# Kernel optimization log

Measured on AMD Instinct MI355X. Metric: run time of the kernel, lower is better.

Reference implementation:

```python
import jax, jax.numpy as jnp
import numpy as np

N = 20000      # nodes
E = 320000     # edges (before self-loops)
IN = 256       # in_channels
HID = 64       # hidden_channels
HEADS = 4      # num_heads
OUT = 64       # out_channels
NEG_SLOPE = 0.2  # GATConv default leaky-relu slope


def setup_inputs() -> dict:
    key = jax.random.key(0)
    ks = jax.random.split(key, 12)
    s = 0.1
    x = jax.random.normal(ks[0], (N, IN), dtype=jnp.float32)
    edge_index = jax.random.randint(ks[1], (2, E), 0, N, dtype=jnp.int64)
    # Layer 1: IN -> HID per head, HEADS heads, concat
    W1 = jax.random.normal(ks[2], (IN, HEADS * HID), dtype=jnp.float32) * s
    a1_src = jax.random.normal(ks[3], (HEADS, HID), dtype=jnp.float32) * s
    a1_dst = jax.random.normal(ks[4], (HEADS, HID), dtype=jnp.float32) * s
    b1 = jnp.zeros((HEADS * HID,), dtype=jnp.float32)
    # Layer 2: HEADS*HID -> OUT, 1 head, no concat
    W2 = jax.random.normal(ks[5], (HEADS * HID, OUT), dtype=jnp.float32) * s
    a2_src = jax.random.normal(ks[6], (1, OUT), dtype=jnp.float32) * s
    a2_dst = jax.random.normal(ks[7], (1, OUT), dtype=jnp.float32) * s
    b2 = jnp.zeros((OUT,), dtype=jnp.float32)
    return {"x": x, "edge_index": edge_index,
            "W1": W1, "a1_src": a1_src, "a1_dst": a1_dst, "b1": b1,
            "W2": W2, "a2_src": a2_src, "a2_dst": a2_dst, "b2": b2}


def _gat_layer(x, src, dst, W, a_src, a_dst, bias, heads, out_c, concat):
    n = x.shape[0]
    h = (x @ W).reshape(n, heads, out_c)                    # [N,H,C]
    e_src = jnp.einsum('nhc,hc->nh', h, a_src)              # [N,H]
    e_dst = jnp.einsum('nhc,hc->nh', h, a_dst)              # [N,H]
    logits = jax.nn.leaky_relu(e_src[src] + e_dst[dst], NEG_SLOPE)  # [E',H]
    # segment softmax over incoming edges of each dst node
    m = jax.ops.segment_max(logits, dst, num_segments=n)    # [N,H]
    p = jnp.exp(logits - m[dst])                            # [E',H]
    z = jax.ops.segment_sum(p, dst, num_segments=n)         # [N,H]
    alpha = p / z[dst]                                      # [E',H]
    out = jax.ops.segment_sum(h[src] * alpha[:, :, None], dst, num_segments=n)
    out = out.reshape(n, heads * out_c) if concat else out.mean(axis=1)
    return out + bias


def reference(x, edge_index, W1, a1_src, a1_dst, b1, W2, a2_src, a2_dst, b2):
    # PyG GATConv adds self-loops by default
    loop = jnp.arange(N, dtype=edge_index.dtype)
    src = jnp.concatenate([edge_index[0], loop])
    dst = jnp.concatenate([edge_index[1], loop])
    h = _gat_layer(x, src, dst, W1, a1_src, a1_dst, b1, HEADS, HID, True)
    h = jax.nn.elu(h)
    # F.dropout defaults training=False -> identity in eval reference
    out = _gat_layer(h, src, dst, W2, a2_src, a2_dst, b2, 1, OUT, False)
    return out
```

## Files before the change

### kernel.cpp

```cpp
#include <hip/hip_runtime.h>
#include <math.h>

#define NEG 0.2f
#define CSTRIDE 64
#define LOG2E 1.4426950408889634f

typedef __attribute__((ext_vector_type(8))) short bf16x8;
typedef __attribute__((ext_vector_type(4))) float f32x4;
typedef unsigned int u32;

__device__ inline float bf2f(unsigned short u) {
    union { unsigned int i; float f; } v; v.i = ((unsigned int)u) << 16; return v.f;
}
__device__ inline unsigned short f2bf(float f) {
    union { float f; unsigned int i; } v; v.f = f;
    unsigned int r = v.i + 0x7FFF + ((v.i >> 16) & 1);
    return (unsigned short)(r >> 16);
}
__device__ inline void unpack8(uint4 hv, float* o) {
    o[0] = bf2f((unsigned short)(hv.x & 0xffffu));
    o[1] = bf2f((unsigned short)(hv.x >> 16));
    o[2] = bf2f((unsigned short)(hv.y & 0xffffu));
    o[3] = bf2f((unsigned short)(hv.y >> 16));
    o[4] = bf2f((unsigned short)(hv.z & 0xffffu));
    o[5] = bf2f((unsigned short)(hv.z >> 16));
    o[6] = bf2f((unsigned short)(hv.w & 0xffffu));
    o[7] = bf2f((unsigned short)(hv.w >> 16));
}
__device__ inline void load_lds16(const unsigned short* g, unsigned short* l) {
    __builtin_amdgcn_global_load_lds((const __attribute__((address_space(1))) u32*)g,
                                     (__attribute__((address_space(3))) u32*)l, 16, 0, 0);
}

__device__ void gemm1_block(int bm, int bn, unsigned short* As, unsigned short* Bs,
                            const unsigned short* __restrict__ A,
                            const unsigned short* __restrict__ Bt,
                            unsigned short* __restrict__ C,
                            const float* __restrict__ a1s, const float* __restrict__ a1d,
                            float* __restrict__ es, float* __restrict__ ed, int M) {
    const int tid = threadIdx.x;
    const int wave = tid >> 6, lane = tid & 63;
    const int wm = (wave >> 1) * 64, wn = (wave & 1) * 64;
    const int lm = lane & 15, kq = lane >> 4;
    const int rA = lane >> 2, cA = (lane & 3) * 8;

    int grA[2], grB[2];
#pragma unroll
    for (int i = 0; i < 2; ++i) {
        int c = wave * 2 + i;
        int gr = bm + c * 16 + rA;
        if (gr >= M) gr = M - 1;
        grA[i] = gr;
        grB[i] = bn + c * 16 + rA;
    }

    auto stage = [&](int t, int b) {
        const int k0 = t * 32;
        const int ka = (k0 < 512) ? k0 : k0 - 512;
#pragma unroll
        for (int i = 0; i < 2; ++i) {
            int c = wave * 2 + i;
            load_lds16(A + (size_t)grA[i] * 512 + ka + cA, As + b * 4096 + c * 512);
            load_lds16(Bt + (size_t)grB[i] * 768 + k0 + cA, Bs + b * 4096 + c * 512);
        }
    };

    f32x4 acc[4][4] = {};
    stage(0, 0);
    stage(1, 1);
    int buf = 0;
    for (int t = 0; t < 24; ++t) {
        if (t < 22) {
            int nb = buf + 2;
            if (nb >= 3) nb -= 3;
            stage(t + 2, nb);
            asm volatile("s_waitcnt vmcnt(8)" ::: "memory");
        } else if (t == 22) {
            asm volatile("s_waitcnt vmcnt(4)" ::: "memory");
        } else {
            asm volatile("s_waitcnt vmcnt(0)" ::: "memory");
        }
        __builtin_amdgcn_s_barrier();
        __builtin_amdgcn_sched_barrier(0);
        bf16x8 af[4], bfr[4];
#pragma unroll
        for (int f = 0; f < 4; ++f) af[f] = *(const bf16x8*)(As + buf * 4096 + (wm + f * 16 + lm) * 32 + kq * 8);
#pragma unroll
        for (int f = 0; f < 4; ++f) bfr[f] = *(const bf16x8*)(Bs + buf * 4096 + (wn + f * 16 + lm) * 32 + kq * 8);
#pragma unroll
        for (int fr = 0; fr < 4; ++fr)
#pragma unroll
            for (int fc = 0; fc < 4; ++fc)
                acc[fr][fc] = __builtin_amdgcn_mfma_f32_16x16x32_bf16(af[fr], bfr[fc], acc[fr][fc], 0, 0, 0);
        __builtin_amdgcn_s_barrier();
        __builtin_amdgcn_sched_barrier(0);
        buf = (buf + 1 == 3) ? 0 : buf + 1;
    }
    const int head = (bn + wn) >> 6;
    float asv[4], adv[4];
#pragma unroll
    for (int fc = 0; fc < 4; ++fc) {
        int ch = fc * 16 + lm;
        asv[fc] = a1s[head * 64 + ch];
        adv[fc] = a1d[head * 64 + ch];
    }
#pragma unroll
    for (int fr = 0; fr < 4; ++fr)
#pragma unroll
        for (int i = 0; i < 4; ++i) {
            int row = bm + wm + fr * 16 + kq * 4 + i;
            float se = 0.f, de = 0.f;
#pragma unroll
            for (int fc = 0; fc < 4; ++fc) {
                float c = acc[fr][fc][i];
                se = fmaf(asv[fc], c, se);
                de = fmaf(adv[fc], c, de);
            }
#pragma unroll
            for (int off = 1; off < 16; off <<= 1) {
                se += __shfl_xor(se, off, 64);
                de += __shfl_xor(de, off, 64);
            }
            if (row < M) {
                if (lm == 0) {
                    es[row * 4 + head] = se * LOG2E;
                    ed[row * 4 + head] = de * LOG2E;
                }
#pragma unroll
                for (int fc = 0; fc < 4; ++fc)
                    C[(size_t)row * 256 + bn + wn + fc * 16 + lm] = f2bf(acc[fr][fc][i]);
            }
        }
}

__global__ __launch_bounds__(256) void pre(const float* __restrict__ x,
                                           const float* __restrict__ W1,
                                           const float* __restrict__ W2,
                                           unsigned short* __restrict__ xs,
                                           unsigned short* __restrict__ Wt1,
                                           unsigned short* __restrict__ Wt2,
                                           int* __restrict__ cnt,
                                           int xb, int wb, int N) {
    int b = blockIdx.x, tid = threadIdx.x;
    if (b < xb) {
        int i = b * 256 + tid;
        if (i >= N * 64) return;
        int e0 = i * 4;
        int node = e0 >> 8, c = e0 & 255;
        float4 f = *(const float4*)(x + e0);
        unsigned short h0 = f2bf(f.x), h1 = f2bf(f.y), h2 = f2bf(f.z), h3 = f2bf(f.w);
        uint2 hi, lo;
        hi.x = (u32)h0 | ((u32)h1 << 16);
        hi.y = (u32)h2 | ((u32)h3 << 16);
        lo.x = (u32)f2bf(f.x - bf2f(h0)) | ((u32)f2bf(f.y - bf2f(h1)) << 16);
        lo.y = (u32)f2bf(f.z - bf2f(h2)) | ((u32)f2bf(f.w - bf2f(h3)) << 16);
        *(uint2*)(xs + (size_t)node * 512 + c) = hi;
        *(uint2*)(xs + (size_t)node * 512 + 256 + c) = lo;
    } else if (b < xb + wb) {
        int i = (b - xb) * 256 + tid;
        const float* W;
        unsigned short* Wt;
        int outc;
        if (i < 256 * 768) { W = W1; Wt = Wt1; outc = 256; }
        else {
            i -= 256 * 768;
            if (i >= 64 * 768) return;
            W = W2; Wt = Wt2; outc = 64;
        }
        int n = i / 768, k = i % 768;
        int ksrc = (k < 256) ? k : (k < 512 ? k - 256 : k - 512);
        float f = W[(size_t)ksrc * outc + n];
        unsigned short h = f2bf(f);
        if (k >= 512) h = f2bf(f - bf2f(h));
        Wt[i] = h;
    } else {
        int i = (b - xb - wb) * 256 + tid;
        if (i < N) cnt[i] = 0;
    }
}

__global__ __launch_bounds__(256) void fused_g1fill(
    int gcnt,
    const unsigned short* __restrict__ A, const unsigned short* __restrict__ Bt,
    unsigned short* __restrict__ C,
    const float* __restrict__ a1s, const float* __restrict__ a1d,
    float* __restrict__ es, float* __restrict__ ed, int M,
    const int* __restrict__ ei, int E,
    int* __restrict__ cnt, int* __restrict__ csr) {
    __shared__ int uni[12288];
    if ((int)blockIdx.x < gcnt) {
        int gid = blockIdx.x;
        unsigned short* sm = (unsigned short*)uni;
        gemm1_block((gid >> 1) * 128, (gid & 1) * 128, sm, sm + 12288,
                    A, Bt, C, a1s, a1d, es, ed, M);
    } else {
        int e = (blockIdx.x - gcnt) * 256 + threadIdx.x;
        if (e < E + M) {
            int s, d;
            if (e < E) { s = ei[e]; d = ei[E + e]; }
            else       { s = d = e - E; }
            int c = atomicAdd(&cnt[d], 1);
            if (c < CSTRIDE) csr[(size_t)d * CSTRIDE + c] = s << 9;
        }
    }
}

__global__ __launch_bounds__(256) void gemm2_scores(const unsigned short* __restrict__ A,
                                                    const unsigned short* __restrict__ Bt,
                                                    unsigned short* __restrict__ C,
                                                    const float* __restrict__ a2s,
                                                    const float* __restrict__ a2d,
                                                    float* __restrict__ es,
                                                    float* __restrict__ ed, int M) {
    __shared__ unsigned short As[3][64 * 32];
    __shared__ unsigned short Bs[3][64 * 32];
    const int tid = threadIdx.x;
    const int bm = blockIdx.x * 64;
    const int wave = tid >> 6, lane = tid & 63;
    const int wm = wave * 16;
    const int lm = lane & 15, kq = lane >> 4;
    const int rA = lane >> 2, cA = (lane & 3) * 8;

    int grA = bm + wave * 16 + rA;
    if (grA >= M) grA = M - 1;
    int grB = wave * 16 + rA;

    auto stage = [&](int t, int b) {
        const int k0 = t * 32;
        const int ka = (k0 < 512) ? k0 : k0 - 512;
        load_lds16(A + (size_t)grA * 512 + ka + cA, &As[b][wave * 512]);
        load_lds16(Bt + (size_t)grB * 768 + k0 + cA, &Bs[b][wave * 512]);
    };

    f32x4 acc[4] = {};
    stage(0, 0);
    stage(1, 1);
    int buf = 0;
    for (int t = 0; t < 24; ++t) {
        if (t < 22) {
            int nb = buf + 2;
            if (nb >= 3) nb -= 3;
            stage(t + 2, nb);
            asm volatile("s_waitcnt vmcnt(4)" ::: "memory");
        } else if (t == 22) {
            asm volatile("s_waitcnt vmcnt(2)" ::: "memory");
        } else {
            asm volatile("s_waitcnt vmcnt(0)" ::: "memory");
        }
        __builtin_amdgcn_s_barrier();
        __builtin_amdgcn_sched_barrier(0);
        bf16x8 af = *(const bf16x8*)(&As[buf][(wm + lm) * 32 + kq * 8]);
        bf16x8 bfr[4];
#pragma unroll
        for (int f = 0; f < 4; ++f) bfr[f] = *(const bf16x8*)(&Bs[buf][(f * 16 + lm) * 32 + kq * 8]);
#pragma unroll
        for (int fc = 0; fc < 4; ++fc)
            acc[fc] = __builtin_amdgcn_mfma_f32_16x16x32_bf16(af, bfr[fc], acc[fc], 0, 0, 0);
        __builtin_amdgcn_s_barrier();
        __builtin_amdgcn_sched_barrier(0);
        buf = (buf + 1 == 3) ? 0 : buf + 1;
    }
    float asv[4], adv[4];
#pragma unroll
    for (int fc = 0; fc < 4; ++fc) {
        int ch = fc * 16 + lm;
        asv[fc] = a2s[ch];
        adv[fc] = a2d[ch];
    }
#pragma unroll
    for (int i = 0; i < 4; ++i) {
        int row = bm + wm + kq * 4 + i;
        float se = 0.f, de = 0.f;
#pragma unroll
        for (int fc = 0; fc < 4; ++fc) {
            float c = acc[fc][i];
            se = fmaf(asv[fc], c, se);
            de = fmaf(adv[fc], c, de);
        }
#pragma unroll
        for (int off = 1; off < 16; off <<= 1) {
            se += __shfl_xor(se, off, 64);
            de += __shfl_xor(de, off, 64);
        }
        if (row < M) {
            if (lm == 0) {
                es[row] = se * LOG2E;
                ed[row] = de * LOG2E;
            }
#pragma unroll
            for (int fc = 0; fc < 4; ++fc)
                C[(size_t)row * 64 + fc * 16 + lm] = f2bf(acc[fc][i]);
        }
    }
}

__global__ __launch_bounds__(256) void agg1(const unsigned short* __restrict__ h,
                                            const int* __restrict__ csr,
                                            const int* __restrict__ cnt,
                                            const float* __restrict__ es,
                                            const float* __restrict__ ed,
                                            const float* __restrict__ b1,
                                            unsigned short* __restrict__ outs, int n) {
    int node = blockIdx.x * 8 + (threadIdx.x >> 5);
    int g = threadIdx.x & 31;
    if (node >= n) return;
    int hh = g >> 3;
    int cb = g * 8;
    int cb2 = cb * 2;
    int hh4 = hh * 4;
    const char* hb = (const char*)h;
    const char* eb = (const char*)es;
    float edst = ed[node * 4 + hh];
    int j0 = node * CSTRIDE;
    int c0 = cnt[node];
    int j1 = j0 + (c0 < CSTRIDE ? c0 : CSTRIDE);
    float z0 = 0.f, z1 = 0.f, z2 = 0.f, z3 = 0.f;
    float a0[8] = {}, a1a[8] = {}, a2a[8] = {}, a3a[8] = {};
    int j = j0;
    for (; j + 4 <= j1; j += 4) {
        int o0 = csr[j], o1 = csr[j + 1], o2 = csr[j + 2], o3 = csr[j + 3];
        uint4 v0 = *(const uint4*)(hb + o0 + cb2);
        uint4 v1 = *(const uint4*)(hb + o1 + cb2);
        uint4 v2 = *(const uint4*)(hb + o2 + cb2);
        uint4 v3 = *(const uint4*)(hb + o3 + cb2);
        float l0 = *(const float*)(eb + (o0 >> 5) + hh4) + edst;
        float l1 = *(const float*)(eb + (o1 >> 5) + hh4) + edst;
        float l2 = *(const float*)(eb + (o2 >> 5) + hh4) + edst;
        float l3 = *(const float*)(eb + (o3 >> 5) + hh4) + edst;
        l0 = (l0 > 0.f) ? l0 : NEG * l0;
        l1 = (l1 > 0.f) ? l1 : NEG * l1;
        l2 = (l2 > 0.f) ? l2 : NEG * l2;
        l3 = (l3 > 0.f) ? l3 : NEG * l3;
        float p0 = exp2f(l0), p1 = exp2f(l1), p2 = exp2f(l2), p3 = exp2f(l3);
        z0 += p0; z1 += p1; z2 += p2; z3 += p3;
        float t[8];
        unpack8(v0, t);
#pragma unroll
        for (int c = 0; c < 8; ++c) a0[c] = fmaf(p0, t[c], a0[c]);
        unpack8(v1, t);
#pragma unroll
        for (int c = 0; c < 8; ++c) a1a[c] = fmaf(p1, t[c], a1a[c]);
        unpack8(v2, t);
#pragma unroll
        for (int c = 0; c < 8; ++c) a2a[c] = fmaf(p2, t[c], a2a[c]);
        unpack8(v3, t);
#pragma unroll
        for (int c = 0; c < 8; ++c) a3a[c] = fmaf(p3, t[c], a3a[c]);
    }
    for (; j < j1; ++j) {
        int o0 = csr[j];
        uint4 v0 = *(const uint4*)(hb + o0 + cb2);
        float l0 = *(const float*)(eb + (o0 >> 5) + hh4) + edst;
        l0 = (l0 > 0.f) ? l0 : NEG * l0;
        float p0 = exp2f(l0);
        z0 += p0;
        float t[8];
        unpack8(v0, t);
#pragma unroll
        for (int c = 0; c < 8; ++c) a0[c] = fmaf(p0, t[c], a0[c]);
    }
    float z = (z0 + z1) + (z2 + z3);
    float inv = 1.f / z;
    float r[8];
    unsigned short qh[8], ql[8];
#pragma unroll
    for (int c = 0; c < 8; ++c) {
        r[c] = ((a0[c] + a1a[c]) + (a2a[c] + a3a[c])) * inv + b1[cb + c];
        r[c] = (r[c] > 0.f) ? r[c] : (__expf(r[c]) - 1.f);
        qh[c] = f2bf(r[c]);
        ql[c] = f2bf(r[c] - bf2f(qh[c]));
    }
    uint4 hiw, low;
    hiw.x = (u32)qh[0] | ((u32)qh[1] << 16);
    hiw.y = (u32)qh[2] | ((u32)qh[3] << 16);
    hiw.z = (u32)qh[4] | ((u32)qh[5] << 16);
    hiw.w = (u32)qh[6] | ((u32)qh[7] << 16);
    low.x = (u32)ql[0] | ((u32)ql[1] << 16);
    low.y = (u32)ql[2] | ((u32)ql[3] << 16);
    low.z = (u32)ql[4] | ((u32)ql[5] << 16);
    low.w = (u32)ql[6] | ((u32)ql[7] << 16);
    *(uint4*)(outs + (size_t)node * 512 + cb) = hiw;
    *(uint4*)(outs + (size_t)node * 512 + 256 + cb) = low;
}

__global__ __launch_bounds__(256) void agg2(const unsigned short* __restrict__ h,
                                            const int* __restrict__ csr,
                                            const int* __restrict__ cnt,
                                            const float* __restrict__ es,
                                            const float* __restrict__ ed,
                                            const float* __restrict__ b2,
                                            float* __restrict__ out, int n) {
    int node = blockIdx.x * 32 + (threadIdx.x >> 3);
    int g = threadIdx.x & 7;
    if (node >= n) return;
    int cb = g * 8;
    int cb2 = cb * 2;
    const char* hb = (const char*)h;
    const char* eb = (const char*)es;
    float edst = ed[node];
    int j0 = node * CSTRIDE;
    int c0 = cnt[node];
    int j1 = j0 + (c0 < CSTRIDE ? c0 : CSTRIDE);
    float z0 = 0.f, z1 = 0.f, z2 = 0.f, z3 = 0.f;
    float a0[8] = {}, a1a[8] = {}, a2a[8] = {}, a3a[8] = {};
    int j = j0;
    for (; j + 4 <= j1; j += 4) {
        int o0 = csr[j], o1 = csr[j + 1], o2 = csr[j + 2], o3 = csr[j + 3];
        uint4 v0 = *(const uint4*)(hb + (o0 >> 2) + cb2);
        uint4 v1 = *(const uint4*)(hb + (o1 >> 2) + cb2);
        uint4 v2 = *(const uint4*)(hb + (o2 >> 2) + cb2);
        uint4 v3 = *(const uint4*)(hb + (o3 >> 2) + cb2);
        float l0 = *(const float*)(eb + (o0 >> 7)) + edst;
        float l1 = *(const float*)(eb + (o1 >> 7)) + edst;
        float l2 = *(const float*)(eb + (o2 >> 7)) + edst;
        float l3 = *(const float*)(eb + (o3 >> 7)) + edst;
        l0 = (l0 > 0.f) ? l0 : NEG * l0;
        l1 = (l1 > 0.f) ? l1 : NEG * l1;
        l2 = (l2 > 0.f) ? l2 : NEG * l2;
        l3 = (l3 > 0.f) ? l3 : NEG * l3;
        float p0 = exp2f(l0), p1 = exp2f(l1), p2 = exp2f(l2), p3 = exp2f(l3);
        z0 += p0; z1 += p1; z2 += p2; z3 += p3;
        float t[8];
        unpack8(v0, t);
#pragma unroll
        for (int c = 0; c < 8; ++c) a0[c] = fmaf(p0, t[c], a0[c]);
        unpack8(v1, t);
#pragma unroll
        for (int c = 0; c < 8; ++c) a1a[c] = fmaf(p1, t[c], a1a[c]);
        unpack8(v2, t);
#pragma unroll
        for (int c = 0; c < 8; ++c) a2a[c] = fmaf(p2, t[c], a2a[c]);
        unpack8(v3, t);
#pragma unroll
        for (int c = 0; c < 8; ++c) a3a[c] = fmaf(p3, t[c], a3a[c]);
    }
    for (; j < j1; ++j) {
        int o0 = csr[j];
        uint4 v0 = *(const uint4*)(hb + (o0 >> 2) + cb2);
        float l0 = *(const float*)(eb + (o0 >> 7)) + edst;
        l0 = (l0 > 0.f) ? l0 : NEG * l0;
        float p0 = exp2f(l0);
        z0 += p0;
        float t[8];
        unpack8(v0, t);
#pragma unroll
        for (int c = 0; c < 8; ++c) a0[c] = fmaf(p0, t[c], a0[c]);
    }
    float z = (z0 + z1) + (z2 + z3);
    float inv = 1.f / z;
    float4 r0, r1;
    r0.x = ((a0[0] + a1a[0]) + (a2a[0] + a3a[0])) * inv + b2[cb + 0];
    r0.y = ((a0[1] + a1a[1]) + (a2a[1] + a3a[1])) * inv + b2[cb + 1];
    r0.z = ((a0[2] + a1a[2]) + (a2a[2] + a3a[2])) * inv + b2[cb + 2];
    r0.w = ((a0[3] + a1a[3]) + (a2a[3] + a3a[3])) * inv + b2[cb + 3];
    r1.x = ((a0[4] + a1a[4]) + (a2a[4] + a3a[4])) * inv + b2[cb + 4];
    r1.y = ((a0[5] + a1a[5]) + (a2a[5] + a3a[5])) * inv + b2[cb + 5];
    r1.z = ((a0[6] + a1a[6]) + (a2a[6] + a3a[6])) * inv + b2[cb + 6];
    r1.w = ((a0[7] + a1a[7]) + (a2a[7] + a3a[7])) * inv + b2[cb + 7];
    *(float4*)(out + (size_t)node * 64 + cb) = r0;
    *(float4*)(out + (size_t)node * 64 + cb + 4) = r1;
}

extern "C" void kernel_launch(void* const* d_in, const int* in_sizes, int n_in,
                              void* d_out, int out_size, void* d_ws, size_t ws_size,
                              hipStream_t stream) {
    const float* x   = (const float*)d_in[0];
    const int*   ei  = (const int*)d_in[1];
    const float* W1  = (const float*)d_in[2];
    const float* a1s = (const float*)d_in[3];
    const float* a1d = (const float*)d_in[4];
    const float* b1  = (const float*)d_in[5];
    const float* W2  = (const float*)d_in[6];
    const float* a2s = (const float*)d_in[7];
    const float* a2d = (const float*)d_in[8];
    const float* b2  = (const float*)d_in[9];
    float* out = (float*)d_out;

    const int N = in_sizes[0] / 256;
    const int E = in_sizes[1] / 2;

    char* p = (char*)d_ws;
    auto take = [&](size_t bytes) {
        char* r = p;
        p += (bytes + 255) & ~(size_t)255;
        return r;
    };
    int* cnt  = (int*)take((size_t)N * 4);
    int* csr  = (int*)take((size_t)N * CSTRIDE * 4);
    unsigned short* hstk = (unsigned short*)take((size_t)N * 512 * 2);
    unsigned short* Wt1  = (unsigned short*)take((size_t)256 * 768 * 2);
    unsigned short* Wt2  = (unsigned short*)take((size_t)64 * 768 * 2);
    unsigned short* h1   = (unsigned short*)take((size_t)N * 256 * 2);
    unsigned short* h2   = (unsigned short*)take((size_t)N * 64 * 2);
    float* es1 = (float*)take((size_t)N * 4 * 4);
    float* ed1 = (float*)take((size_t)N * 4 * 4);
    float* es2 = (float*)take((size_t)N * 4);
    float* ed2 = (float*)take((size_t)N * 4);

    int xb = (N * 64 + 255) / 256;
    int wb = (256 * 768 + 64 * 768 + 255) / 256;
    int zb = (N + 255) / 256;
    pre<<<xb + wb + zb, 256, 0, stream>>>(x, W1, W2, hstk, Wt1, Wt2, cnt, xb, wb, N);

    int GT = 2 * ((N + 127) / 128);
    int eb = (E + N + 255) / 256;
    fused_g1fill<<<GT + eb, 256, 0, stream>>>(GT, hstk, Wt1, h1, a1s, a1d, es1, ed1, N,
                                              ei, E, cnt, csr);

    agg1<<<(N + 7) / 8, 256, 0, stream>>>(h1, csr, cnt, es1, ed1, b1, hstk, N);

    gemm2_scores<<<(N + 63) / 64, 256, 0, stream>>>(hstk, Wt2, h2, a2s, a2d, es2, ed2, N);

    agg2<<<(N + 31) / 32, 256, 0, stream>>>(h2, csr, cnt, es2, ed2, b2, out, N);
}
```

Baseline: 166.5 us.

## Fuse fp32-to-bf16 hi/lo split of x into GEMM1 A-tile staging

The separate pre-pass that converted x into a stacked bf16 hi/lo buffer is removed. GEMM1 now loads fp32 x directly into registers, converts it to bf16 hi or lo on the fly, and writes the result to LDS. The B operand is still loaded with global_load_lds. The pipeline changes from a 3-stage async buffer to 2-stage double buffering with __syncthreads, and LDS use shrinks. This removes a full write and reread of the N×512 bf16 staging buffer, at the cost of redoing the conversion in each of the two column-tile blocks, adding register pressure, and giving less latency hiding.

```diff
diff --git a/kernel.cpp b/kernel.cpp
--- a/kernel.cpp
+++ b/kernel.cpp
@@ -33,7 +33,7 @@
 }
 
 __device__ void gemm1_block(int bm, int bn, unsigned short* As, unsigned short* Bs,
-                            const unsigned short* __restrict__ A,
+                            const float* __restrict__ X,
                             const unsigned short* __restrict__ Bt,
                             unsigned short* __restrict__ C,
                             const float* __restrict__ a1s, const float* __restrict__ a1d,
@@ -54,47 +54,73 @@
         grB[i] = bn + c * 16 + rA;
     }
 
-    auto stage = [&](int t, int b) {
-        const int k0 = t * 32;
-        const int ka = (k0 < 512) ? k0 : k0 - 512;
+    auto loadA = [&](int t, float4 v[2][2]) {
+        const int col = (t * 32) & 255;
+#pragma unroll
+        for (int i = 0; i < 2; ++i) {
+            const float* s = X + (size_t)grA[i] * 256 + col + cA;
+            v[i][0] = *(const float4*)s;
+            v[i][1] = *(const float4*)(s + 4);
+        }
+    };
+    auto writeA = [&](int t, float4 v[2][2], int b) {
+        const bool lo = ((t * 32) & 256) != 0;
 #pragma unroll
         for (int i = 0; i < 2; ++i) {
             int c = wave * 2 + i;
-            load_lds16(A + (size_t)grA[i] * 512 + ka + cA, As + b * 4096 + c * 512);
-            load_lds16(Bt + (size_t)grB[i] * 768 + k0 + cA, Bs + b * 4096 + c * 512);
+            float f[8] = {v[i][0].x, v[i][0].y, v[i][0].z, v[i][0].w,
+                          v[i][1].x, v[i][1].y, v[i][1].z, v[i][1].w};
+            unsigned short o[8];
+#pragma unroll
+            for (int jj = 0; jj < 8; ++jj) {
+                unsigned short hbits = f2bf(f[jj]);
+                o[jj] = lo ? f2bf(f[jj] - bf2f(hbits)) : hbits;
+            }
+            uint4 w;
+            w.x = (u32)o[0] | ((u32)o[1] << 16);
+            w.y = (u32)o[2] | ((u32)o[3] << 16);
+            w.z = (u32)o[4] | ((u32)o[5] << 16);
+            w.w = (u32)o[6] | ((u32)o[7] << 16);
+            *(uint4*)(As + (size_t)b * 4096 + c * 512 + lane * 8) = w;
         }
     };
+    auto stageB = [&](int t, int b) {
+        const int k0 = t * 32;
+#pragma unroll
+        for (int i = 0; i < 2; ++i) {
+            int c = wave * 2 + i;
+            load_lds16(Bt + (size_t)grB[i] * 768 + k0 + cA, Bs + (size_t)b * 4096 + c * 512);
+        }
+    };
 
     f32x4 acc[4][4] = {};
-    stage(0, 0);
-    stage(1, 1);
+    {
+        float4 v0[2][2];
+        loadA(0, v0);
+        stageB(0, 0);
+        writeA(0, v0, 0);
+    }
+    __syncthreads();
     int buf = 0;
     for (int t = 0; t < 24; ++t) {
-        if (t < 22) {
-            int nb = buf + 2;
-            if (nb >= 3) nb -= 3;
-            stage(t + 2, nb);
-            asm volatile("s_waitcnt vmcnt(8)" ::: "memory");
-        } else if (t == 22) {
-            asm volatile("s_waitcnt vmcnt(4)" ::: "memory");
-        } else {
-            asm volatile("s_waitcnt vmcnt(0)" ::: "memory");
-        }
-        __builtin_amdgcn_s_barrier();
-        __builtin_amdgcn_sched_barrier(0);
+        float4 vn[2][2];
+        if (t < 23) {
+            loadA(t + 1, vn);
+            stageB(t + 1, buf ^ 1);
+        }
         bf16x8 af[4], bfr[4];
 #pragma unroll
-        for (int f = 0; f < 4; ++f) af[f] = *(const bf16x8*)(As + buf * 4096 + (wm + f * 16 + lm) * 32 + kq * 8);
-#pragma unroll
-        for (int f = 0; f < 4; ++f) bfr[f] = *(const bf16x8*)(Bs + buf * 4096 + (wn + f * 16 + lm) * 32 + kq * 8);
+        for (int f = 0; f < 4; ++f) af[f] = *(const bf16x8*)(As + (size_t)buf * 4096 + (wm + f * 16 + lm) * 32 + kq * 8);
+#pragma unroll
+        for (int f = 0; f < 4; ++f) bfr[f] = *(const bf16x8*)(Bs + (size_t)buf * 4096 + (wn + f * 16 + lm) * 32 + kq * 8);
 #pragma unroll
         for (int fr = 0; fr < 4; ++fr)
 #pragma unroll
             for (int fc = 0; fc < 4; ++fc)
                 acc[fr][fc] = __builtin_amdgcn_mfma_f32_16x16x32_bf16(af[fr], bfr[fc], acc[fr][fc], 0, 0, 0);
-        __builtin_amdgcn_s_barrier();
-        __builtin_amdgcn_sched_barrier(0);
-        buf = (buf + 1 == 3) ? 0 : buf + 1;
+        if (t < 23) writeA(t + 1, vn, buf ^ 1);
+        __syncthreads();
+        buf ^= 1;
     }
     const int head = (bn + wn) >> 6;
     float asv[4], adv[4];
@@ -133,31 +159,15 @@
         }
 }
 
-__global__ __launch_bounds__(256) void pre(const float* __restrict__ x,
-                                           const float* __restrict__ W1,
+__global__ __launch_bounds__(256) void pre(const float* __restrict__ W1,
                                            const float* __restrict__ W2,
-                                           unsigned short* __restrict__ xs,
                                            unsigned short* __restrict__ Wt1,
                                            unsigned short* __restrict__ Wt2,
                                            int* __restrict__ cnt,
-                                           int xb, int wb, int N) {
+                                           int wb, int N) {
     int b = blockIdx.x, tid = threadIdx.x;
-    if (b < xb) {
+    if (b < wb) {
         int i = b * 256 + tid;
-        if (i >= N * 64) return;
-        int e0 = i * 4;
-        int node = e0 >> 8, c = e0 & 255;
-        float4 f = *(const float4*)(x + e0);
-        unsigned short h0 = f2bf(f.x), h1 = f2bf(f.y), h2 = f2bf(f.z), h3 = f2bf(f.w);
-        uint2 hi, lo;
-        hi.x = (u32)h0 | ((u32)h1 << 16);
-        hi.y = (u32)h2 | ((u32)h3 << 16);
-        lo.x = (u32)f2bf(f.x - bf2f(h0)) | ((u32)f2bf(f.y - bf2f(h1)) << 16);
-        lo.y = (u32)f2bf(f.z - bf2f(h2)) | ((u32)f2bf(f.w - bf2f(h3)) << 16);
-        *(uint2*)(xs + (size_t)node * 512 + c) = hi;
-        *(uint2*)(xs + (size_t)node * 512 + 256 + c) = lo;
-    } else if (b < xb + wb) {
-        int i = (b - xb) * 256 + tid;
         const float* W;
         unsigned short* Wt;
         int outc;
@@ -174,25 +184,25 @@
         if (k >= 512) h = f2bf(f - bf2f(h));
         Wt[i] = h;
     } else {
-        int i = (b - xb - wb) * 256 + tid;
+        int i = (b - wb) * 256 + tid;
         if (i < N) cnt[i] = 0;
     }
 }
 
 __global__ __launch_bounds__(256) void fused_g1fill(
     int gcnt,
-    const unsigned short* __restrict__ A, const unsigned short* __restrict__ Bt,
+    const float* __restrict__ X, const unsigned short* __restrict__ Bt,
     unsigned short* __restrict__ C,
     const float* __restrict__ a1s, const float* __restrict__ a1d,
     float* __restrict__ es, float* __restrict__ ed, int M,
     const int* __restrict__ ei, int E,
     int* __restrict__ cnt, int* __restrict__ csr) {
-    __shared__ int uni[12288];
+    __shared__ int uni[8192];
     if ((int)blockIdx.x < gcnt) {
         int gid = blockIdx.x;
         unsigned short* sm = (unsigned short*)uni;
-        gemm1_block((gid >> 1) * 128, (gid & 1) * 128, sm, sm + 12288,
-                    A, Bt, C, a1s, a1d, es, ed, M);
+        gemm1_block((gid >> 1) * 128, (gid & 1) * 128, sm, sm + 8192,
+                    X, Bt, C, a1s, a1d, es, ed, M);
     } else {
         int e = (blockIdx.x - gcnt) * 256 + threadIdx.x;
         if (e < E + M) {
@@ -497,14 +507,13 @@
     float* es2 = (float*)take((size_t)N * 4);
     float* ed2 = (float*)take((size_t)N * 4);
 
-    int xb = (N * 64 + 255) / 256;
     int wb = (256 * 768 + 64 * 768 + 255) / 256;
     int zb = (N + 255) / 256;
-    pre<<<xb + wb + zb, 256, 0, stream>>>(x, W1, W2, hstk, Wt1, Wt2, cnt, xb, wb, N);
+    pre<<<wb + zb, 256, 0, stream>>>(W1, W2, Wt1, Wt2, cnt, wb, N);
 
     int GT = 2 * ((N + 127) / 128);
     int eb = (E + N + 255) / 256;
-    fused_g1fill<<<GT + eb, 256, 0, stream>>>(GT, hstk, Wt1, h1, a1s, a1d, es1, ed1, N,
+    fused_g1fill<<<GT + eb, 256, 0, stream>>>(GT, x, Wt1, h1, a1s, a1d, es1, ed1, N,
                                               ei, E, cnt, csr);
 
     agg1<<<(N + 7) / 8, 256, 0, stream>>>(h1, csr, cnt, es1, ed1, b1, hstk, N);
```

Result: slower. 178.9 us (+7.4%).
